# Optimization experiments

Measured on AMD Instinct MI355X. Metric: run time of the kernel, lower is better.

The kernel has to match this reference:

```python
import jax, jax.numpy as jnp
import numpy as np

ORDER = 3
NUM_CONTROL_POINTS = 8
NUM_CHANNELS = 64
BATCH = 262144
EPS = 1e-8


def setup_inputs() -> dict:
    key = jax.random.key(0)
    kx, kc = jax.random.split(key)
    x = jax.random.normal(kx, (BATCH, NUM_CHANNELS), dtype=jnp.float32)
    control_points = jax.random.normal(kc, (NUM_CHANNELS, NUM_CONTROL_POINTS), dtype=jnp.float32) * 0.1
    return {"x": x, "control_points": control_points}


def _bspline_basis(xc, knots, order):
    """Iterative Cox-de Boor. xc: [..., 1]; returns [..., num_control_points]."""
    # degree-0: N_{i,0} = 1 if knots[i] <= x < knots[i+1]
    N = ((knots[:-1] <= xc) & (xc < knots[1:])).astype(xc.dtype)  # [..., n_knots-1]
    for k in range(1, order + 1):
        d1 = knots[k:-1] - knots[:-(k + 1)]      # knots[i+k]   - knots[i]
        d2 = knots[k + 1:] - knots[1:-k]         # knots[i+k+1] - knots[i+1]
        safe1 = jnp.where(d1 > EPS, d1, 1.0)
        safe2 = jnp.where(d2 > EPS, d2, 1.0)
        t1 = jnp.where(d1 > EPS, (xc - knots[:-(k + 1)]) / safe1, 0.0) * N[..., :-1]
        t2 = jnp.where(d2 > EPS, (knots[k + 1:] - xc) / safe2, 0.0) * N[..., 1:]
        N = t1 + t2
    return N


def reference(x, control_points):
    order = ORDER
    P = control_points.shape[1]
    knots = jnp.linspace(-1.0, 1.0, P + order + 1, dtype=x.dtype)
    xc = jnp.clip(x, -0.99, 0.99)[..., None]          # [B, C, 1]
    basis = _bspline_basis(xc, knots, order)           # [B, C, P]
    # result = sum_i control_points[:, i] * N_{i,order}(x)
    return jnp.einsum('bci,ci->bc', basis, control_points)
```

## Files before the change

### kernel.cpp

```cpp
#include <hip/hip_runtime.h>


constexpr int CH  = 64;
constexpr int PCP = 8;
constexpr int NJ  = 11;
constexpr int TBL = CH * NJ;

__global__ __launch_bounds__(256) void bspline_kan_kernel(
    const float* __restrict__ x,
    const float* __restrict__ cp,
    float* __restrict__ out,
    int n4)
{
    __shared__ float4 tbl[TBL];

    for (int t = threadIdx.x; t < TBL; t += 256) {
        int c = t / NJ;
        int j = t - c * NJ;
        float p[4];
#pragma unroll
        for (int r = 0; r < 4; ++r) {
            int i = j - 3 + r;
            p[r] = (i >= 0 && i < PCP) ? cp[c * PCP + i] : 0.0f;
        }
        float4 a;
        a.x = (p[0] + 4.0f * p[1] + p[2]) * (1.0f / 6.0f);
        a.y = (p[2] - p[0]) * 0.5f;
        a.z = (p[0] - 2.0f * p[1] + p[2]) * 0.5f;
        a.w = (p[3] - p[0] + 3.0f * (p[1] - p[2])) * (1.0f / 6.0f);
        tbl[t] = a;
    }
    __syncthreads();

    const float inv_h = 5.5f;

    int idx    = blockIdx.x * blockDim.x + threadIdx.x;
    int stride = gridDim.x * blockDim.x;
    const float4* __restrict__ x4 = (const float4*)x;
    float4* __restrict__ o4 = (float4*)out;

    for (int i = idx; i < n4; i += stride) {
        float4 xv = x4[i];
        int base_c = (i << 2) & (CH - 1);
        float xs[4] = {xv.x, xv.y, xv.z, xv.w};
        float r[4];
#pragma unroll
        for (int e = 0; e < 4; ++e) {
            float xx = fminf(fmaxf(xs[e], -0.99f), 0.99f);
            float fz = (xx + 1.0f) * inv_h;
            float fj = floorf(fz);
            int j = (int)fj;
            j = max(0, min(j, NJ - 1));
            float u = fz - (float)j;
            float4 a = tbl[(base_c + e) * NJ + j];
            r[e] = fmaf(fmaf(fmaf(a.w, u, a.z), u, a.y), u, a.x);
        }
        float4 ov = {r[0], r[1], r[2], r[3]};
        o4[i] = ov;
    }
}

extern "C" void kernel_launch(void* const* d_in, const int* in_sizes, int n_in,
                              void* d_out, int out_size, void* d_ws, size_t ws_size,
                              hipStream_t stream) {
    const float* x  = (const float*)d_in[0];
    const float* cp = (const float*)d_in[1];
    float* out = (float*)d_out;

    int n4 = in_sizes[0] / 4;
    bspline_kan_kernel<<<2048, 256, 0, stream>>>(x, cp, out, n4);
}
```

Measured before the change: 113.3 us.

## Split LDS table into SoA arrays, add nontemporal IO and 2x unroll

Stores the spline coefficients as four separate scalar LDS arrays instead of one float4 array, which is meant to reduce LDS bank conflicts on the gathered lookups. The channel row offsets are hoisted out of the loop because the stride keeps the channel fixed. Global loads and stores become nontemporal, and each thread handles two float4s per iteration for more memory-level parallelism. The explicit j clamp and the floor call are dropped, which relies on the input clamp keeping the index in range. A thread now issues four scalar LDS reads per element where it previously issued one vector read.

```diff
diff --git a/kernel.cpp b/kernel.cpp
--- a/kernel.cpp
+++ b/kernel.cpp
@@ -1,10 +1,25 @@
 #include <hip/hip_runtime.h>
 
+
+typedef float fvec4 __attribute__((ext_vector_type(4)));
 
 constexpr int CH  = 64;
 constexpr int PCP = 8;
 constexpr int NJ  = 11;
 constexpr int TBL = CH * NJ;
+
+__device__ __forceinline__ float eval_elem(float v, int row,
+                                           const float* __restrict__ c0,
+                                           const float* __restrict__ c1,
+                                           const float* __restrict__ c2,
+                                           const float* __restrict__ c3) {
+    float xx = fminf(fmaxf(v, -0.99f), 0.99f);
+    float fz = fmaf(xx, 5.5f, 5.5f);
+    int   j  = (int)fz;
+    float u  = fz - (float)j;
+    int   o  = row + j;
+    return fmaf(fmaf(fmaf(c3[o], u, c2[o]), u, c1[o]), u, c0[o]);
+}
 
 __global__ __launch_bounds__(256) void bspline_kan_kernel(
     const float* __restrict__ x,
@@ -12,7 +27,7 @@
     float* __restrict__ out,
     int n4)
 {
-    __shared__ float4 tbl[TBL];
+    __shared__ float c0[TBL], c1[TBL], c2[TBL], c3[TBL];
 
     for (int t = threadIdx.x; t < TBL; t += 256) {
         int c = t / NJ;
@@ -23,40 +38,43 @@
             int i = j - 3 + r;
             p[r] = (i >= 0 && i < PCP) ? cp[c * PCP + i] : 0.0f;
         }
-        float4 a;
-        a.x = (p[0] + 4.0f * p[1] + p[2]) * (1.0f / 6.0f);
-        a.y = (p[2] - p[0]) * 0.5f;
-        a.z = (p[0] - 2.0f * p[1] + p[2]) * 0.5f;
-        a.w = (p[3] - p[0] + 3.0f * (p[1] - p[2])) * (1.0f / 6.0f);
-        tbl[t] = a;
+        c0[t] = (p[0] + 4.0f * p[1] + p[2]) * (1.0f / 6.0f);
+        c1[t] = (p[2] - p[0]) * 0.5f;
+        c2[t] = (p[0] - 2.0f * p[1] + p[2]) * 0.5f;
+        c3[t] = (p[3] - p[0] + 3.0f * (p[1] - p[2])) * (1.0f / 6.0f);
     }
     __syncthreads();
 
-    const float inv_h = 5.5f;
+    const fvec4* __restrict__ x4 = (const fvec4*)x;
+    fvec4* __restrict__ o4 = (fvec4*)out;
 
-    int idx    = blockIdx.x * blockDim.x + threadIdx.x;
-    int stride = gridDim.x * blockDim.x;
-    const float4* __restrict__ x4 = (const float4*)x;
-    float4* __restrict__ o4 = (float4*)out;
+    int idx    = blockIdx.x * 256 + threadIdx.x;
+    int stride = gridDim.x * 256;
 
-    for (int i = idx; i < n4; i += stride) {
-        float4 xv = x4[i];
-        int base_c = (i << 2) & (CH - 1);
-        float xs[4] = {xv.x, xv.y, xv.z, xv.w};
-        float r[4];
-#pragma unroll
-        for (int e = 0; e < 4; ++e) {
-            float xx = fminf(fmaxf(xs[e], -0.99f), 0.99f);
-            float fz = (xx + 1.0f) * inv_h;
-            float fj = floorf(fz);
-            int j = (int)fj;
-            j = max(0, min(j, NJ - 1));
-            float u = fz - (float)j;
-            float4 a = tbl[(base_c + e) * NJ + j];
-            r[e] = fmaf(fmaf(fmaf(a.w, u, a.z), u, a.y), u, a.x);
-        }
-        float4 ov = {r[0], r[1], r[2], r[3]};
-        o4[i] = ov;
+    int base_c = (idx << 2) & (CH - 1);
+    int row0 = base_c * NJ;
+    int row1 = row0 + NJ;
+    int row2 = row0 + 2 * NJ;
+    int row3 = row0 + 3 * NJ;
+
+    for (int i = idx; i < n4; i += 2 * stride) {
+        int i2 = i + stride;
+        bool has2 = (i2 < n4);
+        fvec4 xa = __builtin_nontemporal_load(&x4[i]);
+        fvec4 xb = has2 ? __builtin_nontemporal_load(&x4[i2]) : xa;
+
+        fvec4 ra, rb;
+        ra.x = eval_elem(xa.x, row0, c0, c1, c2, c3);
+        ra.y = eval_elem(xa.y, row1, c0, c1, c2, c3);
+        ra.z = eval_elem(xa.z, row2, c0, c1, c2, c3);
+        ra.w = eval_elem(xa.w, row3, c0, c1, c2, c3);
+        rb.x = eval_elem(xb.x, row0, c0, c1, c2, c3);
+        rb.y = eval_elem(xb.y, row1, c0, c1, c2, c3);
+        rb.z = eval_elem(xb.z, row2, c0, c1, c2, c3);
+        rb.w = eval_elem(xb.w, row3, c0, c1, c2, c3);
+
+        __builtin_nontemporal_store(ra, &o4[i]);
+        if (has2) __builtin_nontemporal_store(rb, &o4[i2]);
     }
 }
 
```

Result: slower. 119.0 us (+5.1%).
